# Kernel tuning notes

Measured on AMD Instinct MI355X. Metric: run time of the kernel, lower is better.

## Reference

```python
import jax, jax.numpy as jnp
import numpy as np
from jax import lax

C, S, Q = 20, 8, 16          # n_class, n_support, n_query
IMW, IMH, CH = 84, 84, 3     # image width, height, channels
CNT = 17.0                   # 1 aug + 8 same-class + 8 adversarial pair terms (loop break logic with S=8)

def _conv(x, k, b):
    return lax.conv_general_dilated(x, k, (1, 1), 'SAME',
                                    dimension_numbers=('NHWC', 'HWIO', 'NHWC')) + b

def _pool(x):
    return lax.reduce_window(x, -jnp.inf, lax.max, (1, 2, 2, 1), (1, 2, 2, 1), 'VALID')

def _d2(a, b):
    # calc_euclidian_dists: MEAN of squared differences over feature dim
    return jnp.mean((a - b) ** 2, axis=-1)

def _encoder(x, p):
    (k1, b1, k2, b2, k3, b3, k4, b4, k5, b5, k6, b6, k7, b7, k8, b8,
     g1, be1, g2, be2) = p
    x = _conv(x, k1, b1); x = _conv(x, k2, b2); x = _conv(x, k3, b3); x = _conv(x, k4, b4)
    x = _pool(jax.nn.relu(g1 * x + be1))
    x = _conv(x, k5, b5); x = _conv(x, k6, b6); x = _conv(x, k7, b7); x = _conv(x, k8, b8)
    x = _pool(jax.nn.relu(g2 * x + be2))
    return x.reshape(x.shape[0], -1)

def _pro_encoder(x, p, Wm):
    # same layers, each layer output scaled by W[i] (the `self.W[i] * layer` intent)
    (k1, b1, k2, b2, k3, b3, k4, b4, k5, b5, k6, b6, k7, b7, k8, b8,
     g1, be1, g2, be2) = p
    x = Wm[0] * _conv(x, k1, b1); x = Wm[1] * _conv(x, k2, b2)
    x = Wm[2] * _conv(x, k3, b3); x = Wm[3] * _conv(x, k4, b4)
    x = Wm[4] * (g1 * x + be1); x = Wm[5] * jax.nn.relu(x); x = Wm[6] * _pool(x)
    x = Wm[7] * _conv(x, k5, b5); x = Wm[8] * _conv(x, k6, b6)
    x = Wm[9] * _conv(x, k7, b7); x = Wm[10] * _conv(x, k8, b8)
    x = Wm[11] * (g2 * x + be2); x = Wm[12] * jax.nn.relu(x); x = Wm[13] * _pool(x)
    return Wm[14] * x.reshape(x.shape[0], -1)

def setup_inputs():
    key = jax.random.key(0)
    ks = jax.random.split(key, 24)
    def kern(k, cin):
        return jax.random.normal(k, (3, 3, cin, 16), jnp.float32) * 0.05
    inp = {
        'support': jax.random.normal(ks[0], (C, S, IMW, IMH, CH), jnp.float32),
        'query':   jax.random.normal(ks[1], (C, Q, IMW, IMH, CH), jnp.float32),
        'k1': kern(ks[2], CH)}
    for i in range(2, 9):
        inp['k%d' % i] = kern(ks[1 + i], 16)
    for i in range(1, 9):
        inp['b%d' % i] = jax.random.normal(ks[9 + i], (16,), jnp.float32) * 0.01
    inp['g1'] = jnp.ones((16,), jnp.float32)
    inp['be1'] = jnp.zeros((16,), jnp.float32)
    inp['g2'] = jnp.ones((16,), jnp.float32)
    inp['be2'] = jnp.zeros((16,), jnp.float32)
    inp['Wm'] = jax.random.normal(ks[20], (19,), jnp.float32)
    return inp

def _forward(support, query, p, Wm):
    n_class, n_support = support.shape[0], support.shape[1]
    n_query = query.shape[1]
    cat = jnp.concatenate([support.reshape(-1, IMW, IMH, CH),
                           query.reshape(-1, IMW, IMH, CH)], axis=0)
    z = _encoder(cat, p)
    D = z.shape[-1]
    z1 = z[:n_class * n_support].reshape(n_class, n_support, D)
    # tf.image.flip_left_right flips the second-to-last (width) axis of each image
    z_aug = _encoder(jnp.flip(support, axis=-2).reshape(-1, IMW, IMH, CH), p)
    z_aug = z_aug.reshape(n_class, n_support, D)
    d_aug = _d2(z1, z_aug) ** 2                                       # [C,S]
    # same-class pairwise terms: with S=8 the loop adds all 8 supports then breaks
    pos = jnp.sum(_d2(z1[:, :, None, :], z1[:, None, :, :]) ** 2, axis=2)
    z_adv = jnp.roll(z1, -1, axis=0)                                  # adversarial class (c+1)%C
    neg = jnp.sum(_d2(z1[:, :, None, :], z_adv[:, None, :, :]) ** 2, axis=2)
    uns_loss = jnp.sum((d_aug + pos - neg) / CNT + 0.5)
    zp = _pro_encoder(cat, p, Wm)
    protos = zp[:n_class * n_support].reshape(n_class, n_support, D).mean(axis=1)
    zq = zp[n_class * n_support:]
    dists = _d2(zq[:, None, :], protos[None, :, :])                   # [C*Q, C]
    log_p = jax.nn.log_softmax(-dists, axis=-1).reshape(n_class, n_query, n_class)
    y = jnp.tile(jnp.arange(n_class)[:, None], (1, n_query))
    ce = -jnp.mean(jnp.take_along_axis(log_p, y[:, :, None], axis=-1))
    loss = ce + uns_loss
    acc = jnp.mean((jnp.argmax(log_p, axis=-1) == y).astype(jnp.float32))
    return loss, acc

def reference(support, query, k1, k2, k3, k4, k5, k6, k7, k8,
              b1, b2, b3, b4, b5, b6, b7, b8, g1, be1, g2, be2, Wm):
    p = (k1, b1, k2, b2, k3, b3, k4, b4, k5, b5, k6, b6, k7, b7, k8, b8,
         g1, be1, g2, be2)
    return _forward(support, query, p, Wm)
```

## Files before the change

kernel.cpp:

```cpp
#include <hip/hip_runtime.h>
#include <math.h>


typedef __attribute__((ext_vector_type(8))) short bf16x8;
typedef __attribute__((ext_vector_type(8))) unsigned short u16x8;
typedef __attribute__((ext_vector_type(4))) float f32x4;
typedef unsigned short u16;
typedef unsigned int u32;

#define PIX84 (84 * 84)
#define D     (21 * 21 * 16)
#define WF_LAYER 3072
#define WF_C1 (7 * WF_LAYER)

__device__ __forceinline__ float bf2f(u16 v) {
    union { u32 i; float f; } c; c.i = ((u32)v) << 16; return c.f;
}
__device__ __forceinline__ u16 f2bf(float f) {
    union { float f; u32 i; } c; c.f = f;
    u32 r = c.i + 0x7fffu + ((c.i >> 16) & 1u);
    return (u16)(r >> 16);
}
__device__ __forceinline__ u32 pack2(float a, float b) {
    union { __bf16 h[2]; u32 u; } p;
    p.h[0] = (__bf16)a; p.h[1] = (__bf16)b;
    return p.u;
}

__device__ __forceinline__ bf16x8 ld_bf16x8_a8(const char* p) {
    union { uint2 q[2]; bf16x8 v; } u;
    u.q[0] = *(const uint2*)(p);
    u.q[1] = *(const uint2*)(p + 8);
    return u.v;
}

__device__ __forceinline__ float blockReduceSum(float v) {
    __shared__ float red[8];
    #pragma unroll
    for (int o = 32; o > 0; o >>= 1) v += __shfl_down(v, o, 64);
    const int lane = threadIdx.x & 63, wid = threadIdx.x >> 6;
    __syncthreads();
    if (lane == 0) red[wid] = v;
    __syncthreads();
    float r = 0.f;
    if (threadIdx.x == 0) {
        const int nw = (blockDim.x + 63) >> 6;
        for (int i = 0; i < nw; ++i) r += red[i];
    }
    return r;
}

__global__ void prep_weights(const float* __restrict__ k1, const float* __restrict__ k2,
                             const float* __restrict__ k3, const float* __restrict__ k4,
                             const float* __restrict__ k5, const float* __restrict__ k6,
                             const float* __restrict__ k7, const float* __restrict__ k8,
                             u16* __restrict__ wf)
{
    const int idx = blockIdx.x * 256 + threadIdx.x;
    if (idx < WF_C1) {
        const int j = idx & 7, lane = (idx >> 3) & 63, r = idx >> 9;
        const int s = r % 6, L = r / 6;
        const float* ks[7] = { k2, k3, k4, k5, k6, k7, k8 };
        const int co = lane & 15, g = lane >> 4;
        const int k = g * 8 + j;
        const int t = k >> 4, ci = k & 15;
        float v = 0.f;
        if (t == 0)      v = ks[L][(s * 16 + ci) * 16 + co];
        else if (s >= 3) v = ks[L][((s + 3) * 16 + ci) * 16 + co];
        wf[idx] = f2bf(v);
    } else if (idx < WF_C1 + 1024) {
        const int t = idx - WF_C1;
        const int j = t & 7, lane = (t >> 3) & 63, m = t >> 9;
        const int co = lane & 15, g = lane >> 4;
        const int k = g * 8 + j;
        const int dh  = (m == 0) ? (k >> 4) : 2;
        const int rem = (m == 0) ? (k & 15) : k;
        const int dw = rem >> 2, ci = rem & 3;
        const float v = (rem < 12 && ci < 3) ? k1[((dh * 3 + dw) * 3 + ci) * 16 + co] : 0.f;
        wf[idx] = f2bf(v);
    }
}

template <int W, int LW, int MAXT, int HALF>
__device__ __forceinline__ void conv_layer(char* buf, const u16* wfL,
                                           const float* bias, float scale,
                                           int nrows, int dro, int lane, int wv)
{
    const int g = lane >> 4, col = lane & 15;
    bf16x8 wfr[6];
    #pragma unroll
    for (int s = 0; s < 6; ++s) wfr[s] = ((const bf16x8*)wfL)[s * 64 + lane];
    const float4 bv = *(const float4*)(bias + g * 4);
    const float c0 = bv.x * scale, c1 = bv.y * scale;
    const float c2 = bv.z * scale, c3 = bv.w * scale;
    const int NPX = nrows * W;
    const int TC = (NPX + 15) >> 4;
    const int t0 = wv * MAXT;
    const int rb_const = (g & 1) * HALF + (g >> 1) * (LW * 16);
    const int w2r = ((g >> 1) * HALF + (g & 1) * 8 + (dro * LW + 1) * 16) - rb_const;

    f32x4 acc[MAXT];
    int raddr[MAXT];
    #pragma unroll
    for (int u = 0; u < MAXT; ++u) {
        const int t = t0 + u;
        if (t < TC) {
            const int px = t * 16 + col;
            const int p = (px < NPX) ? px : 0;
            const int j = p / W, w = p - j * W;
            const int ra = rb_const + (j * LW + w) * 16;
            raddr[u] = ra;
            const char* rb = buf + ra;
            f32x4 a = { 0.f, 0.f, 0.f, 0.f };
            a = __builtin_amdgcn_mfma_f32_16x16x32_bf16(wfr[0], *(const bf16x8*)(rb),                a, 0, 0, 0);
            a = __builtin_amdgcn_mfma_f32_16x16x32_bf16(wfr[1], *(const bf16x8*)(rb + 16),           a, 0, 0, 0);
            a = __builtin_amdgcn_mfma_f32_16x16x32_bf16(wfr[2], *(const bf16x8*)(rb + 32),           a, 0, 0, 0);
            a = __builtin_amdgcn_mfma_f32_16x16x32_bf16(wfr[3], *(const bf16x8*)(rb + LW * 16),      a, 0, 0, 0);
            a = __builtin_amdgcn_mfma_f32_16x16x32_bf16(wfr[4], *(const bf16x8*)(rb + LW * 16 + 16), a, 0, 0, 0);
            a = __builtin_amdgcn_mfma_f32_16x16x32_bf16(wfr[5], *(const bf16x8*)(rb + LW * 16 + 32), a, 0, 0, 0);
            acc[u] = a;
        }
    }
    __syncthreads();
    #pragma unroll
    for (int u = 0; u < MAXT; ++u) {
        const int t = t0 + u;
        if (t < TC) {
            const int px = t * 16 + col;
            if (px < NPX) {
                const u32 lo = pack2(fmaf(acc[u][0], scale, c0), fmaf(acc[u][1], scale, c1));
                const u32 hi = pack2(fmaf(acc[u][2], scale, c2), fmaf(acc[u][3], scale, c3));
                *(uint2*)(buf + raddr[u] + w2r) = make_uint2(lo, hi);
            }
        }
    }
    __syncthreads();
}

#define HALF1 (20 * 86 * 16 + 16)
__global__ __launch_bounds__(512) void stage1_kernel(
    const float* __restrict__ sup, const float* __restrict__ qry,
    const float* __restrict__ b1,
    const u16* __restrict__ wf,
    const float* __restrict__ b2, const float* __restrict__ b3,
    const float* __restrict__ b4,
    const float* __restrict__ g1, const float* __restrict__ be1,
    const float* __restrict__ Wm,
    u16* __restrict__ s1out)
{
    __shared__ char buf[2 * HALF1];
    __shared__ u16 stag[(22 * 86 + 2) * 4];
    const int img = blockIdx.x / 6, bb = blockIdx.x % 6;
    const int R0 = 14 * bb;
    const int tid = threadIdx.x, lane = tid & 63, wv = tid >> 6;
    const bool pro = img >= 320;

    const float* src;
    bool flip = false;
    if (img < 160) src = sup + (size_t)img * (PIX84 * 3);
    else if (img < 320) { src = sup + (size_t)(img - 160) * (PIX84 * 3); flip = true; }
    else {
        const int m = img - 320;
        src = (m < 160) ? sup + (size_t)m * (PIX84 * 3)
                        : qry + (size_t)(m - 160) * (PIX84 * 3);
    }
    const float s1 = pro ? Wm[0] : 1.f, s2 = pro ? Wm[1] : 1.f;
    const float s3 = pro ? Wm[2] : 1.f, s4 = pro ? Wm[3] : 1.f;
    const float pre = pro ? Wm[4] : 1.f, rs = pro ? Wm[5] : 1.f;
    const float post = pro ? Wm[6] : 1.f;

    for (int i = tid; i < 40; i += 512) {
        const int P = (i >> 1) * 86 + ((i & 1) ? 85 : 0);
        *(uint4*)(buf + P * 16) = make_uint4(0, 0, 0, 0);
        *(uint4*)(buf + HALF1 + P * 16) = make_uint4(0, 0, 0, 0);
    }

    for (int p = tid; p < 22 * 86; p += 512) {
        const int r = p / 86, c = p - r * 86;
        const int hin = R0 - 4 + r, win = c - 1;
        u32 lo = 0, hi = 0;
        if ((unsigned)hin < 84u && (unsigned)win < 84u) {
            const int wsrc = flip ? (83 - win) : win;
            const float* ip = src + ((size_t)(hin * 84 + wsrc)) * 3;
            lo = pack2(ip[0], ip[1]);
            hi = pack2(ip[2], 0.f);
        }
        *(uint2*)((char*)stag + (size_t)p * 8) = make_uint2(lo, hi);
    }
    __syncthreads();

    {
        const int g = lane >> 4, col = lane & 15;
        const bf16x8 wA0 = ((const bf16x8*)(wf + WF_C1))[lane];
        const bf16x8 wA1 = ((const bf16x8*)(wf + WF_C1))[64 + lane];
        const float4 bv = *(const float4*)(b1 + g * 4);
        const int off0 = ((g >> 1) * 86 + (g & 1) * 2) * 8;
        const int off1 = (2 * 86 + (g & 1) * 2) * 8;
        const int wb_const = (g >> 1) * HALF1 + (g & 1) * 8;
        for (int t = wv; t < 105; t += 8) {
            const int p = t * 16 + col;
            const int ri = p / 84, w = p - ri * 84;
            const int base = (ri * 86 + w) * 8;
            const bf16x8 B0 = ld_bf16x8_a8((const char*)stag + base + off0);
            const bf16x8 B1 = ld_bf16x8_a8((const char*)stag + base + off1);
            f32x4 a = { 0.f, 0.f, 0.f, 0.f };
            a = __builtin_amdgcn_mfma_f32_16x16x32_bf16(wA0, B0, a, 0, 0, 0);
            a = __builtin_amdgcn_mfma_f32_16x16x32_bf16(wA1, B1, a, 0, 0, 0);
            const int h = R0 - 3 + ri;
            const float sc = ((unsigned)h < 84u) ? s1 : 0.f;
            const u32 lo = pack2((a[0] + bv.x) * sc, (a[1] + bv.y) * sc);
            const u32 hi = pack2((a[2] + bv.z) * sc, (a[3] + bv.w) * sc);
            *(uint2*)(buf + wb_const + (ri * 86 + (w + 1)) * 16) = make_uint2(lo, hi);
        }
    }
    __syncthreads();

    conv_layer<84, 86, 12, HALF1>(buf, wf,                b2, s2, 18, 0, lane, wv);
    conv_layer<84, 86, 11, HALF1>(buf, wf + WF_LAYER,     b3, s3, 16, 0, lane, wv);
    conv_layer<84, 86, 10, HALF1>(buf, wf + 2 * WF_LAYER, b4, s4, 14, 0, lane, wv);

    const u32 uPRS = __float_as_uint(pre * rs);
    const float AR = post * rs;
    for (int e = tid; e < 7 * 42 * 2; e += 512) {
        const int hf = e & 1;
        const int pc = (e >> 1) % 42, pr = (e >> 1) / 42;
        const char* hb = buf + hf * HALF1;
        const int P0 = (2 * pr) * 86 + (2 * pc + 1);
        const u16x8 v00 = *(const u16x8*)(hb + P0 * 16);
        const u16x8 v01 = *(const u16x8*)(hb + (P0 + 1) * 16);
        const u16x8 v10 = *(const u16x8*)(hb + (P0 + 86) * 16);
        const u16x8 v11 = *(const u16x8*)(hb + (P0 + 87) * 16);
        float o[8];
        #pragma unroll
        for (int c = 0; c < 8; ++c) {
            const int ch = hf * 8 + c;
            const float x0 = bf2f(v00[c]), x1 = bf2f(v01[c]);
            const float x2 = bf2f(v10[c]), x3 = bf2f(v11[c]);
            const float mx = fmaxf(fmaxf(fmaxf(x0, x1), x2), x3);
            const float mn = fminf(fminf(fminf(x0, x1), x2), x3);
            const float gch = g1[ch];
            const bool dn = ((__float_as_uint(gch) ^ uPRS) >> 31) != 0;
            const float m = dn ? mn : mx;
            o[c] = AR * fmaxf(0.f, fmaf(pre * gch, m, pre * be1[ch]));
        }
        uint4 ov;
        ov.x = pack2(o[0], o[1]);
        ov.y = pack2(o[2], o[3]);
        ov.z = pack2(o[4], o[5]);
        ov.w = pack2(o[6], o[7]);
        *(uint4*)(s1out + (size_t)img * 28224 +
                  ((size_t)(7 * bb + pr) * 42 + pc) * 16 + hf * 8) = ov;
    }
}

#define LW2   46
#define HALF2 (44 * LW2 * 16 + 16)
__global__ __launch_bounds__(512) void stage2_kernel(
    const u16* __restrict__ s1in, const u16* __restrict__ wf,
    const float* __restrict__ b5, const float* __restrict__ b6,
    const float* __restrict__ b7, const float* __restrict__ b8,
    const float* __restrict__ g2, const float* __restrict__ be2,
    const float* __restrict__ Wm,
    float* __restrict__ z, float* __restrict__ zp)
{
    __shared__ char buf[2 * HALF2];
    const int img = blockIdx.x;
    const int tid = threadIdx.x, lane = tid & 63, wv = tid >> 6;
    const bool pro = img >= 320;
    const float s5 = pro ? Wm[7] : 1.f, s6 = pro ? Wm[8] : 1.f;
    const float s7 = pro ? Wm[9] : 1.f, s8 = pro ? Wm[10] : 1.f;
    const float pre = pro ? Wm[11] : 1.f, rs = pro ? Wm[12] : 1.f;
    const float post = pro ? (Wm[13] * Wm[14]) : 1.f;

    for (int i = tid; i < 44 * 44; i += 512) {
        const int r = i / 44, c = i - r * 44;
        if (r == 0 || r == 43 || c == 0 || c == 43) {
            const int P = r * LW2 + c;
            *(uint4*)(buf + P * 16) = make_uint4(0, 0, 0, 0);
            *(uint4*)(buf + HALF2 + P * 16) = make_uint4(0, 0, 0, 0);
        }
    }
    const u16* ip = s1in + (size_t)img * 28224;
    for (int cix = tid; cix < 42 * 42 * 2; cix += 512) {
        const int Pi = cix >> 1, hf = cix & 1;
        const int r = Pi / 42, c = Pi - r * 42;
        const uint4 v = *(const uint4*)(ip + (size_t)cix * 8);
        *(uint4*)(buf + hf * HALF2 + ((r + 1) * LW2 + (c + 1)) * 16) = v;
    }
    __syncthreads();

    conv_layer<42, LW2, 14, HALF2>(buf, wf + 3 * WF_LAYER, b5, s5, 42, 1, lane, wv);
    conv_layer<42, LW2, 14, HALF2>(buf, wf + 4 * WF_LAYER, b6, s6, 42, 1, lane, wv);
    conv_layer<42, LW2, 14, HALF2>(buf, wf + 5 * WF_LAYER, b7, s7, 42, 1, lane, wv);
    conv_layer<42, LW2, 14, HALF2>(buf, wf + 6 * WF_LAYER, b8, s8, 42, 1, lane, wv);

    float* outp = pro ? (zp + (size_t)(img - 320) * D) : (z + (size_t)img * D);
    const u32 uPRS = __float_as_uint(pre * rs);
    const float AR = post * rs;
    for (int e = tid; e < 21 * 21 * 2; e += 512) {
        const int hf = e & 1;
        const int pc = (e >> 1) % 21, pr = (e >> 1) / 21;
        const char* hb = buf + hf * HALF2;
        const int P0 = (2 * pr + 1) * LW2 + (2 * pc + 1);
        const u16x8 v00 = *(const u16x8*)(hb + P0 * 16);
        const u16x8 v01 = *(const u16x8*)(hb + (P0 + 1) * 16);
        const u16x8 v10 = *(const u16x8*)(hb + (P0 + LW2) * 16);
        const u16x8 v11 = *(const u16x8*)(hb + (P0 + LW2 + 1) * 16);
        float o[8];
        #pragma unroll
        for (int c = 0; c < 8; ++c) {
            const int ch = hf * 8 + c;
            const float x0 = bf2f(v00[c]), x1 = bf2f(v01[c]);
            const float x2 = bf2f(v10[c]), x3 = bf2f(v11[c]);
            const float mx = fmaxf(fmaxf(fmaxf(x0, x1), x2), x3);
            const float mn = fminf(fminf(fminf(x0, x1), x2), x3);
            const float gch = g2[ch];
            const bool dn = ((__float_as_uint(gch) ^ uPRS) >> 31) != 0;
            const float m = dn ? mn : mx;
            o[c] = AR * fmaxf(0.f, fmaf(pre * gch, m, pre * be2[ch]));
        }
        float* op = outp + ((size_t)(pr * 21 + pc)) * 16 + hf * 8;
        *(float4*)op = make_float4(o[0], o[1], o[2], o[3]);
        *(float4*)(op + 4) = make_float4(o[4], o[5], o[6], o[7]);
    }
}

__global__ void pairs_kernel(const float* __restrict__ z,
                             float* __restrict__ within, float* __restrict__ cross,
                             float* __restrict__ aug)
{
    const int bid = blockIdx.x;
    const float *u, *v;
    float* dst;
    if (bid < 1280) {
        const int c = bid / 64, i = (bid % 64) / 8, j = bid % 8;
        u = z + (size_t)(c * 8 + i) * D;
        v = z + (size_t)(c * 8 + j) * D;
        dst = within + bid;
    } else if (bid < 2560) {
        const int t = bid - 1280;
        const int c = t / 64, i = (t % 64) / 8, j = t % 8;
        const int c2 = (c + 1) % 20;
        u = z + (size_t)(c * 8 + i) * D;
        v = z + (size_t)(c2 * 8 + j) * D;
        dst = cross + t;
    } else {
        const int t = bid - 2560;
        u = z + (size_t)t * D;
        v = z + (size_t)(160 + t) * D;
        dst = aug + t;
    }
    const float4* u4 = (const float4*)u;
    const float4* v4 = (const float4*)v;
    float s = 0.f;
    for (int d = threadIdx.x; d < D / 4; d += 256) {
        const float4 a = u4[d], b = v4[d];
        const float dx = a.x - b.x, dy = a.y - b.y, dz = a.z - b.z, dw = a.w - b.w;
        s += dx * dx + dy * dy + dz * dz + dw * dw;
    }
    s = blockReduceSum(s);
    if (threadIdx.x == 0) {
        const float m = s / (float)D;
        *dst = m * m;
    }
}

__global__ void protos_kernel(const float* __restrict__ zp, float* __restrict__ protos)
{
    const int idx = blockIdx.x * 256 + threadIdx.x;
    if (idx >= 20 * D) return;
    const int c = idx / D, d = idx % D;
    float s = 0.f;
    #pragma unroll
    for (int i = 0; i < 8; ++i) s += zp[(size_t)(c * 8 + i) * D + d];
    protos[idx] = s * 0.125f;
}

__global__ void dists_kernel(const float* __restrict__ zq, const float* __restrict__ protos,
                             float* __restrict__ dists)
{
    const int q = blockIdx.x / 20, c = blockIdx.x % 20;
    const float4* u4 = (const float4*)(zq + (size_t)q * D);
    const float4* v4 = (const float4*)(protos + (size_t)c * D);
    float s = 0.f;
    for (int d = threadIdx.x; d < D / 4; d += 256) {
        const float4 a = u4[d], b = v4[d];
        const float dx = a.x - b.x, dy = a.y - b.y, dz = a.z - b.z, dw = a.w - b.w;
        s += dx * dx + dy * dy + dz * dz + dw * dw;
    }
    s = blockReduceSum(s);
    if (threadIdx.x == 0) dists[blockIdx.x] = s / (float)D;
}

__global__ void final_kernel(const float* __restrict__ dists,
                             const float* __restrict__ within,
                             const float* __restrict__ cross,
                             const float* __restrict__ aug,
                             float* __restrict__ out)
{
    float ce = 0.f, accv = 0.f, uns = 0.f;
    for (int r = threadIdx.x; r < 320; r += 256) {
        const float* dr = dists + r * 20;
        const int y = r / 16;
        float dmin = dr[0];
        int amin = 0;
        float m = -dr[0];
        #pragma unroll
        for (int j = 1; j < 20; ++j) {
            if (dr[j] < dmin) { dmin = dr[j]; amin = j; }
            m = fmaxf(m, -dr[j]);
        }
        float se = 0.f;
        #pragma unroll
        for (int j = 0; j < 20; ++j) se += expf(-dr[j] - m);
        const float lse = m + logf(se);
        ce += dr[y] + lse;
        accv += (amin == y) ? 1.0f : 0.0f;
    }
    for (int i = threadIdx.x; i < 1280; i += 256) uns += within[i] - cross[i];
    for (int i = threadIdx.x; i < 160; i += 256) uns += aug[i];

    ce = blockReduceSum(ce);
    accv = blockReduceSum(accv);
    uns = blockReduceSum(uns);
    if (threadIdx.x == 0) {
        out[0] = ce / 320.0f + uns / 17.0f + 80.0f;
        out[1] = accv / 320.0f;
    }
}

extern "C" void kernel_launch(void* const* d_in, const int* in_sizes, int n_in,
                              void* d_out, int out_size, void* d_ws, size_t ws_size,
                              hipStream_t stream)
{
    (void)in_sizes; (void)n_in; (void)out_size; (void)ws_size;
    const float* sup = (const float*)d_in[0];
    const float* qry = (const float*)d_in[1];
    const float* K[8]; for (int i = 0; i < 8; ++i) K[i] = (const float*)d_in[2 + i];
    const float* B[8]; for (int i = 0; i < 8; ++i) B[i] = (const float*)d_in[10 + i];
    const float* g1  = (const float*)d_in[18];
    const float* be1 = (const float*)d_in[19];
    const float* g2  = (const float*)d_in[20];
    const float* be2 = (const float*)d_in[21];
    const float* Wm  = (const float*)d_in[22];
    float* out = (float*)d_out;

    size_t off = 0;
    auto alloc = [&](size_t bytes) -> void* {
        void* p = (char*)d_ws + off;
        off += (bytes + 255) & ~(size_t)255;
        return p;
    };
    u16*   wf     = (u16*)alloc((size_t)(WF_C1 + 1024) * 2);
    u16*   s1out  = (u16*)alloc((size_t)800 * 42 * 42 * 16 * 2);
    float* z      = (float*)alloc((size_t)320 * D * 4);
    float* zp     = (float*)alloc((size_t)480 * D * 4);
    float* within = (float*)alloc(1280 * 4);
    float* crossb = (float*)alloc(1280 * 4);
    float* augb   = (float*)alloc(160 * 4);
    float* protos = (float*)alloc((size_t)20 * D * 4);
    float* dist   = (float*)alloc(6400 * 4);

    prep_weights<<<(WF_C1 + 1024 + 255) / 256, 256, 0, stream>>>(
        K[0], K[1], K[2], K[3], K[4], K[5], K[6], K[7], wf);

    stage1_kernel<<<800 * 6, 512, 0, stream>>>(sup, qry, B[0], wf,
                                               B[1], B[2], B[3], g1, be1, Wm, s1out);
    stage2_kernel<<<800, 512, 0, stream>>>(s1out, wf, B[4], B[5], B[6], B[7],
                                           g2, be2, Wm, z, zp);

    pairs_kernel<<<2720, 256, 0, stream>>>(z, within, crossb, augb);
    protos_kernel<<<(20 * D + 255) / 256, 256, 0, stream>>>(zp, protos);
    dists_kernel<<<6400, 256, 0, stream>>>(zp + (size_t)160 * D, protos, dist);
    final_kernel<<<1, 256, 0, stream>>>(dist, within, crossb, augb, out);
}
```

Baseline: 295.3 us.

## Repack conv weights to 5 MFMAs per tile and split stage2 into row halves

Conv weight fragments are re-laid out so the 9 taps x 16 channels fit in 5 K=32 MFMA steps instead of 6, removing the zero-padded taps. Each tap group now reads at its own shared-memory offset, and the output writes zeros outside valid rows so borders are handled explicitly. Stage2 is split into two blocks per image, each covering half the rows plus a halo, with a smaller shared buffer. This doubles the grid for better occupancy at the cost of recomputing overlapping halo rows.

Result: no change. 295.5 us (+0.1%).

```diff
diff --git a/kernel.cpp b/kernel.cpp
--- a/kernel.cpp
+++ b/kernel.cpp
@@ -10,7 +10,7 @@
 
 #define PIX84 (84 * 84)
 #define D     (21 * 21 * 16)
-#define WF_LAYER 3072
+#define WF_LAYER 2560
 #define WF_C1 (7 * WF_LAYER)
 
 __device__ __forceinline__ float bf2f(u16 v) {
@@ -59,14 +59,13 @@
     const int idx = blockIdx.x * 256 + threadIdx.x;
     if (idx < WF_C1) {
         const int j = idx & 7, lane = (idx >> 3) & 63, r = idx >> 9;
-        const int s = r % 6, L = r / 6;
+        const int m = r % 5, L = r / 5;
         const float* ks[7] = { k2, k3, k4, k5, k6, k7, k8 };
         const int co = lane & 15, g = lane >> 4;
-        const int k = g * 8 + j;
-        const int t = k >> 4, ci = k & 15;
-        float v = 0.f;
-        if (t == 0)      v = ks[L][(s * 16 + ci) * 16 + co];
-        else if (s >= 3) v = ks[L][((s + 3) * 16 + ci) * 16 + co];
+        const int gg = g >> 1, h = g & 1;
+        const int tap = gg ? (m + 5) : m;
+        const int ci = h * 8 + j;
+        const float v = (tap < 9) ? ks[L][(tap * 16 + ci) * 16 + co] : 0.f;
         wf[idx] = f2bf(v);
     } else if (idx < WF_C1 + 1024) {
         const int t = idx - WF_C1;
@@ -84,23 +83,29 @@
 template <int W, int LW, int MAXT, int HALF>
 __device__ __forceinline__ void conv_layer(char* buf, const u16* wfL,
                                            const float* bias, float scale,
-                                           int nrows, int dro, int lane, int wv)
-{
-    const int g = lane >> 4, col = lane & 15;
-    bf16x8 wfr[6];
+                                           int nrows, int v0, int v1,
+                                           int lane, int wv)
+{
+    const int g = lane >> 4, col = lane & 15, gg = g >> 1, h = g & 1;
+    bf16x8 wfr[5];
     #pragma unroll
-    for (int s = 0; s < 6; ++s) wfr[s] = ((const bf16x8*)wfL)[s * 64 + lane];
+    for (int s = 0; s < 5; ++s) wfr[s] = ((const bf16x8*)wfL)[s * 64 + lane];
     const float4 bv = *(const float4*)(bias + g * 4);
     const float c0 = bv.x * scale, c1 = bv.y * scale;
     const float c2 = bv.z * scale, c3 = bv.w * scale;
     const int NPX = nrows * W;
     const int TC = (NPX + 15) >> 4;
     const int t0 = wv * MAXT;
-    const int rb_const = (g & 1) * HALF + (g >> 1) * (LW * 16);
-    const int w2r = ((g >> 1) * HALF + (g & 1) * 8 + (dro * LW + 1) * 16) - rb_const;
+    const int C0 = h * HALF + (gg ? (LW + 2)      : 0        ) * 16;
+    const int C1 = h * HALF + (gg ? (2 * LW)      : 1        ) * 16;
+    const int C2 = h * HALF + (gg ? (2 * LW + 1)  : 2        ) * 16;
+    const int C3 = h * HALF + (gg ? (2 * LW + 2)  : LW       ) * 16;
+    const int C4 = h * HALF + (gg ? (LW + 2)      : (LW + 1) ) * 16;
+    const int wb = gg * HALF + h * 8 + 16;
 
     f32x4 acc[MAXT];
     int raddr[MAXT];
+    u32 vmask = 0;
     #pragma unroll
     for (int u = 0; u < MAXT; ++u) {
         const int t = t0 + u;
@@ -108,16 +113,16 @@
             const int px = t * 16 + col;
             const int p = (px < NPX) ? px : 0;
             const int j = p / W, w = p - j * W;
-            const int ra = rb_const + (j * LW + w) * 16;
+            const int ra = (j * LW + w) * 16;
             raddr[u] = ra;
+            if ((px < NPX) && (j >= v0) && (j < v1)) vmask |= (1u << u);
             const char* rb = buf + ra;
             f32x4 a = { 0.f, 0.f, 0.f, 0.f };
-            a = __builtin_amdgcn_mfma_f32_16x16x32_bf16(wfr[0], *(const bf16x8*)(rb),                a, 0, 0, 0);
-            a = __builtin_amdgcn_mfma_f32_16x16x32_bf16(wfr[1], *(const bf16x8*)(rb + 16),           a, 0, 0, 0);
-            a = __builtin_amdgcn_mfma_f32_16x16x32_bf16(wfr[2], *(const bf16x8*)(rb + 32),           a, 0, 0, 0);
-            a = __builtin_amdgcn_mfma_f32_16x16x32_bf16(wfr[3], *(const bf16x8*)(rb + LW * 16),      a, 0, 0, 0);
-            a = __builtin_amdgcn_mfma_f32_16x16x32_bf16(wfr[4], *(const bf16x8*)(rb + LW * 16 + 16), a, 0, 0, 0);
-            a = __builtin_amdgcn_mfma_f32_16x16x32_bf16(wfr[5], *(const bf16x8*)(rb + LW * 16 + 32), a, 0, 0, 0);
+            a = __builtin_amdgcn_mfma_f32_16x16x32_bf16(wfr[0], *(const bf16x8*)(rb + C0), a, 0, 0, 0);
+            a = __builtin_amdgcn_mfma_f32_16x16x32_bf16(wfr[1], *(const bf16x8*)(rb + C1), a, 0, 0, 0);
+            a = __builtin_amdgcn_mfma_f32_16x16x32_bf16(wfr[2], *(const bf16x8*)(rb + C2), a, 0, 0, 0);
+            a = __builtin_amdgcn_mfma_f32_16x16x32_bf16(wfr[3], *(const bf16x8*)(rb + C3), a, 0, 0, 0);
+            a = __builtin_amdgcn_mfma_f32_16x16x32_bf16(wfr[4], *(const bf16x8*)(rb + C4), a, 0, 0, 0);
             acc[u] = a;
         }
     }
@@ -128,9 +133,12 @@
         if (t < TC) {
             const int px = t * 16 + col;
             if (px < NPX) {
-                const u32 lo = pack2(fmaf(acc[u][0], scale, c0), fmaf(acc[u][1], scale, c1));
-                const u32 hi = pack2(fmaf(acc[u][2], scale, c2), fmaf(acc[u][3], scale, c3));
-                *(uint2*)(buf + raddr[u] + w2r) = make_uint2(lo, hi);
+                u32 lo = 0, hi = 0;
+                if ((vmask >> u) & 1u) {
+                    lo = pack2(fmaf(acc[u][0], scale, c0), fmaf(acc[u][1], scale, c1));
+                    hi = pack2(fmaf(acc[u][2], scale, c2), fmaf(acc[u][3], scale, c3));
+                }
+                *(uint2*)(buf + raddr[u] + wb) = make_uint2(lo, hi);
             }
         }
     }
@@ -206,8 +214,8 @@
             f32x4 a = { 0.f, 0.f, 0.f, 0.f };
             a = __builtin_amdgcn_mfma_f32_16x16x32_bf16(wA0, B0, a, 0, 0, 0);
             a = __builtin_amdgcn_mfma_f32_16x16x32_bf16(wA1, B1, a, 0, 0, 0);
-            const int h = R0 - 3 + ri;
-            const float sc = ((unsigned)h < 84u) ? s1 : 0.f;
+            const int hrow = R0 - 3 + ri;
+            const float sc = ((unsigned)hrow < 84u) ? s1 : 0.f;
             const u32 lo = pack2((a[0] + bv.x) * sc, (a[1] + bv.y) * sc);
             const u32 hi = pack2((a[2] + bv.z) * sc, (a[3] + bv.w) * sc);
             *(uint2*)(buf + wb_const + (ri * 86 + (w + 1)) * 16) = make_uint2(lo, hi);
@@ -215,9 +223,12 @@
     }
     __syncthreads();
 
-    conv_layer<84, 86, 12, HALF1>(buf, wf,                b2, s2, 18, 0, lane, wv);
-    conv_layer<84, 86, 11, HALF1>(buf, wf + WF_LAYER,     b3, s3, 16, 0, lane, wv);
-    conv_layer<84, 86, 10, HALF1>(buf, wf + 2 * WF_LAYER, b4, s4, 14, 0, lane, wv);
+    conv_layer<84, 86, 12, HALF1>(buf, wf,                b2, s2, 18,
+                                  (2 - R0 > 0) ? 2 - R0 : 0, (86 - R0 < 18) ? 86 - R0 : 18, lane, wv);
+    conv_layer<84, 86, 11, HALF1>(buf, wf + WF_LAYER,     b3, s3, 16,
+                                  (1 - R0 > 0) ? 1 - R0 : 0, (85 - R0 < 16) ? 85 - R0 : 16, lane, wv);
+    conv_layer<84, 86, 10, HALF1>(buf, wf + 2 * WF_LAYER, b4, s4, 14,
+                                  0,                         (84 - R0 < 14) ? 84 - R0 : 14, lane, wv);
 
     const u32 uPRS = __float_as_uint(pre * rs);
     const float AR = post * rs;
@@ -254,7 +265,8 @@
 }
 
 #define LW2   46
-#define HALF2 (44 * LW2 * 16 + 16)
+#define NR2   30
+#define HALF2 (NR2 * LW2 * 16 + 16)
 __global__ __launch_bounds__(512) void stage2_kernel(
     const u16* __restrict__ s1in, const u16* __restrict__ wf,
     const float* __restrict__ b5, const float* __restrict__ b6,
@@ -264,7 +276,9 @@
     float* __restrict__ z, float* __restrict__ zp)
 {
     __shared__ char buf[2 * HALF2];
-    const int img = blockIdx.x;
+    const int img = blockIdx.x >> 1, hb2 = blockIdx.x & 1;
+    const int nc8 = hb2 ? 20 : 22;
+    const int R0in = hb2 ? 18 : -4;
     const int tid = threadIdx.x, lane = tid & 63, wv = tid >> 6;
     const bool pro = img >= 320;
     const float s5 = pro ? Wm[7] : 1.f, s6 = pro ? Wm[8] : 1.f;
@@ -272,36 +286,44 @@
     const float pre = pro ? Wm[11] : 1.f, rs = pro ? Wm[12] : 1.f;
     const float post = pro ? (Wm[13] * Wm[14]) : 1.f;
 
-    for (int i = tid; i < 44 * 44; i += 512) {
+    const u16* ip = s1in + (size_t)img * 28224;
+    for (int i = tid; i < NR2 * 44; i += 512) {
         const int r = i / 44, c = i - r * 44;
-        if (r == 0 || r == 43 || c == 0 || c == 43) {
-            const int P = r * LW2 + c;
-            *(uint4*)(buf + P * 16) = make_uint4(0, 0, 0, 0);
-            *(uint4*)(buf + HALF2 + P * 16) = make_uint4(0, 0, 0, 0);
-        }
-    }
-    const u16* ip = s1in + (size_t)img * 28224;
-    for (int cix = tid; cix < 42 * 42 * 2; cix += 512) {
-        const int Pi = cix >> 1, hf = cix & 1;
-        const int r = Pi / 42, c = Pi - r * 42;
-        const uint4 v = *(const uint4*)(ip + (size_t)cix * 8);
-        *(uint4*)(buf + hf * HALF2 + ((r + 1) * LW2 + (c + 1)) * 16) = v;
-    }
-    __syncthreads();
-
-    conv_layer<42, LW2, 14, HALF2>(buf, wf + 3 * WF_LAYER, b5, s5, 42, 1, lane, wv);
-    conv_layer<42, LW2, 14, HALF2>(buf, wf + 4 * WF_LAYER, b6, s6, 42, 1, lane, wv);
-    conv_layer<42, LW2, 14, HALF2>(buf, wf + 5 * WF_LAYER, b7, s7, 42, 1, lane, wv);
-    conv_layer<42, LW2, 14, HALF2>(buf, wf + 6 * WF_LAYER, b8, s8, 42, 1, lane, wv);
+        const int gr = R0in + r;
+        const int P = r * LW2 + c;
+        uint4 v0 = make_uint4(0, 0, 0, 0), v1 = v0;
+        if (c >= 1 && c <= 42 && gr >= 0 && gr < 42) {
+            const u16* q = ip + ((size_t)(gr * 42 + (c - 1))) * 16;
+            v0 = *(const uint4*)q;
+            v1 = *(const uint4*)(q + 8);
+        }
+        *(uint4*)(buf + P * 16) = v0;
+        *(uint4*)(buf + HALF2 + P * 16) = v1;
+    }
+    __syncthreads();
+
+    {
+        const int n1 = nc8 + 6, n2 = nc8 + 4, n3 = nc8 + 2, n4 = nc8;
+        int a0, a1;
+        a0 = -R0in - 1; if (a0 < 0) a0 = 0; a1 = 41 - R0in; if (a1 > n1) a1 = n1;
+        conv_layer<42, LW2, 10, HALF2>(buf, wf + 3 * WF_LAYER, b5, s5, n1, a0, a1, lane, wv);
+        a0 = -R0in - 2; if (a0 < 0) a0 = 0; a1 = 40 - R0in; if (a1 > n2) a1 = n2;
+        conv_layer<42, LW2, 10, HALF2>(buf, wf + 4 * WF_LAYER, b6, s6, n2, a0, a1, lane, wv);
+        a0 = -R0in - 3; if (a0 < 0) a0 = 0; a1 = 39 - R0in; if (a1 > n3) a1 = n3;
+        conv_layer<42, LW2, 10, HALF2>(buf, wf + 5 * WF_LAYER, b7, s7, n3, a0, a1, lane, wv);
+        a0 = -R0in - 4; if (a0 < 0) a0 = 0; a1 = 38 - R0in; if (a1 > n4) a1 = n4;
+        conv_layer<42, LW2, 10, HALF2>(buf, wf + 6 * WF_LAYER, b8, s8, n4, a0, a1, lane, wv);
+    }
 
     float* outp = pro ? (zp + (size_t)(img - 320) * D) : (z + (size_t)img * D);
     const u32 uPRS = __float_as_uint(pre * rs);
     const float AR = post * rs;
-    for (int e = tid; e < 21 * 21 * 2; e += 512) {
+    const int np = nc8 >> 1;
+    for (int e = tid; e < np * 21 * 2; e += 512) {
         const int hf = e & 1;
         const int pc = (e >> 1) % 21, pr = (e >> 1) / 21;
         const char* hb = buf + hf * HALF2;
-        const int P0 = (2 * pr + 1) * LW2 + (2 * pc + 1);
+        const int P0 = (2 * pr) * LW2 + (2 * pc + 1);
         const u16x8 v00 = *(const u16x8*)(hb + P0 * 16);
         const u16x8 v01 = *(const u16x8*)(hb + (P0 + 1) * 16);
         const u16x8 v10 = *(const u16x8*)(hb + (P0 + LW2) * 16);
@@ -319,7 +341,7 @@
             const float m = dn ? mn : mx;
             o[c] = AR * fmaxf(0.f, fmaf(pre * gch, m, pre * be2[ch]));
         }
-        float* op = outp + ((size_t)(pr * 21 + pc)) * 16 + hf * 8;
+        float* op = outp + ((size_t)((hb2 * 11 + pr) * 21 + pc)) * 16 + hf * 8;
         *(float4*)op = make_float4(o[0], o[1], o[2], o[3]);
         *(float4*)(op + 4) = make_float4(o[4], o[5], o[6], o[7]);
     }
@@ -466,8 +488,8 @@
 
     stage1_kernel<<<800 * 6, 512, 0, stream>>>(sup, qry, B[0], wf,
                                                B[1], B[2], B[3], g1, be1, Wm, s1out);
-    stage2_kernel<<<800, 512, 0, stream>>>(s1out, wf, B[4], B[5], B[6], B[7],
-                                           g2, be2, Wm, z, zp);
+    stage2_kernel<<<1600, 512, 0, stream>>>(s1out, wf, B[4], B[5], B[6], B[7],
+                                            g2, be2, Wm, z, zp);
 
     pairs_kernel<<<2720, 256, 0, stream>>>(z, within, crossb, augb);
     protos_kernel<<<(20 * D + 255) / 256, 256, 0, stream>>>(zp, protos);
```
